# Kernel optimization log

Hardware: AMD Instinct MI355X
Metric: run time of the kernel (lower is better)

The kernel has to match this reference:

```python
import jax, jax.numpy as jnp
import numpy as np

# static config (mirrors init_kwargs)
F_T, S = 8, 24            # video_shape = (F_T, S, S)
K, DIL = 3, 1             # kernel_size, dilation (same for all 3 axes)
HEADS, DHEAD, DIM = 8, 64, 512
INNER = HEADS * DHEAD
PAD = DIL * (K - 1)       # causal: pad 2 at the FRONT of each spatial axis
KJ = K ** 3               # 27 neighbors per query
N_VID = F_T * S * S       # 4608 video tokens


def causal_pad(t):
    # t: [B, D, F, S, S] -> pad front of f/h/w axes (torch F.pad (PAD*?,0) causal layout)
    return jnp.pad(t, ((0, 0), (0, 0), (PAD, 0), (PAD, 0), (PAD, 0)))


def unfold3d(t):
    # torch unfoldNd equivalent. t: [B, D, F+PAD, S+PAD, S+PAD]
    # returns [B, N_VID, KJ, D]; kernel offsets ordered (kf, kh, kw) w fastest,
    # matching torch unfold's channel-major / kernel-minor layout after the
    # rearrange 'b (d j) i -> b i j d'.
    sl = []
    for i in range(K):
        for j in range(K):
            for kk in range(K):
                sl.append(t[:, :, i * DIL:i * DIL + F_T,
                                  j * DIL:j * DIL + S,
                                  kk * DIL:kk * DIL + S])
    u = jnp.stack(sl, axis=2)                      # [B, D, KJ, F, S, S]
    B, D = t.shape[0], t.shape[1]
    u = u.reshape(B, D, KJ, N_VID)
    return jnp.transpose(u, (0, 3, 2, 1))          # [B, N_VID, KJ, D]


def make_mask():
    # True where the neighbor falls into zero padding (out-of-range / future under causal pad)
    ones = jnp.ones((1, 1, F_T, S, S), jnp.float32)
    u = unfold3d(causal_pad(ones))[0, :, :, 0]     # [N_VID, KJ]
    m = u == 0.0
    return jnp.pad(m, ((0, 0), (1, 0)), constant_values=False)  # bos col never masked


def stable_softmax(t, alpha=32.0 ** 2):
    t = t / alpha
    t = t - jax.lax.stop_gradient(jnp.max(t, axis=-1, keepdims=True))
    return jax.nn.softmax(t * alpha, axis=-1)


def setup_inputs() -> dict:
    key = jax.random.key(0)
    ks = jax.random.split(key, 9)
    return {
        "x": jax.random.normal(ks[0], (1, N_VID + 1, DIM), jnp.float32),
        "Wq": jax.random.normal(ks[1], (DIM, INNER), jnp.float32) * 0.02,
        "Wkv": jax.random.normal(ks[2], (DIM, 2 * INNER), jnp.float32) * 0.02,
        "W_th": jax.random.normal(ks[3], (HEADS, HEADS), jnp.float32) * 0.2,
        "Wout": jax.random.normal(ks[4], (INNER, DIM), jnp.float32) * 0.02,
        "bout": jax.random.normal(ks[5], (DIM,), jnp.float32) * 0.02,
        "ax1": jax.random.normal(ks[6], (K, HEADS), jnp.float32),
        "ax2": jax.random.normal(ks[7], (K, HEADS), jnp.float32),
        "ax3": jax.random.normal(ks[8], (K, HEADS), jnp.float32),
    }


def reference(x, Wq, Wkv, W_th, Wout, bout, ax1, ax2, ax3):
    b, n, _ = x.shape                       # b=1, n = 1 + N_VID (no extra padding)
    h, d = HEADS, DHEAD
    scale = d ** -0.5

    q = x @ Wq
    k, v = jnp.split(x @ Wkv, 2, axis=-1)

    def to_heads(t):  # 'b n (h d) -> (b h) n d'
        return t.reshape(b, n, h, d).transpose(0, 2, 1, 3).reshape(b * h, n, d)

    q, k, v = map(to_heads, (q, k, v))
    q = q[:, 1:] * scale                    # drop bos query
    k_bos, v_bos = k[:, :1], v[:, :1]       # [bh, 1, d]
    k, v = k[:, 1:], v[:, 1:]

    def to_vid(t):  # 'b (f h w) d -> b d f h w'
        return t.reshape(b * h, F_T, S, S, d).transpose(0, 4, 1, 2, 3)

    ku = unfold3d(causal_pad(to_vid(k)))    # [bh, N, KJ, d]
    vu = unfold3d(causal_pad(to_vid(v)))
    N = ku.shape[1]

    kb = jnp.broadcast_to(k_bos[:, :, None, :], (b * h, N, 1, d))
    vb = jnp.broadcast_to(v_bos[:, :, None, :], (b * h, N, 1, d))
    ku = jnp.concatenate([kb, ku], axis=2)  # [bh, N, KJ+1, d]
    vu = jnp.concatenate([vb, vu], axis=2)

    sim = jnp.einsum('bid,bijd->bij', q, ku)                 # [bh, N, KJ+1]

    # axial relative position bias over the 3x3x3 kernel, pad 0 for bos column
    rel = (ax1[:, None, None, :] + ax2[None, :, None, :] + ax3[None, None, :, :])
    rel = rel.reshape(KJ, h)                                 # [27, h]
    bias = jnp.pad(rel.T[:, None, :], ((0, 0), (0, 0), (1, 0)))  # [h, 1, KJ+1]

    sim = sim.reshape(b, h, N, KJ + 1) + bias[None]
    mask = make_mask()                                       # [N, KJ+1]
    sim = jnp.where(mask[None, None], -jnp.finfo(sim.dtype).max, sim)

    attn = stable_softmax(sim)                               # [b, h, N, KJ+1]
    attn = jnp.einsum('hg,bgij->bhij', W_th, attn)           # talking heads 1x1 conv

    out = jnp.einsum('bhij,bhijd->bhid', attn, vu.reshape(b, h, N, KJ + 1, d))
    out = jnp.concatenate([v_bos.reshape(b, h, 1, d), out], axis=2)  # re-attach bos value
    out = out.transpose(0, 2, 1, 3).reshape(b, n, h * d)     # '(b h) n d -> b n (h d)'
    return out @ Wout + bout
```

## Files before the change

### kernel.cpp

```cpp
#include <hip/hip_runtime.h>
#include <hip/hip_bf16.h>


constexpr int TFR   = 8;
constexpr int SDIM  = 24;
constexpr int NVID  = TFR * SDIM * SDIM;
constexpr int NTOK  = NVID + 1;
constexpr int NH    = 8;
constexpr int DM    = 512;
constexpr int NJ    = 28;

typedef __attribute__((ext_vector_type(8))) short bf16x8;
typedef __attribute__((ext_vector_type(8))) unsigned short ushort8;
typedef __attribute__((ext_vector_type(4))) float f32x4;

typedef const __attribute__((address_space(1))) unsigned int* gas_ptr;
typedef __attribute__((address_space(3))) unsigned int* las_ptr;

__device__ __forceinline__ float bf2f(unsigned short u) {
    return __uint_as_float((unsigned)u << 16);
}
__device__ __forceinline__ unsigned short f2bf(float f) {
    __hip_bfloat16 h = __float2bfloat16(f);
    return reinterpret_cast<unsigned short&>(h);
}

__global__ __launch_bounds__(256)
void prep_w(const float* __restrict__ Wq, const float* __restrict__ Wkv,
            const float* __restrict__ Wout,
            __hip_bfloat16* __restrict__ Wqkvt, __hip_bfloat16* __restrict__ Woutt)
{
    __shared__ float t[32][33];
    const int tid = threadIdx.x;
    int tb = blockIdx.x;
    const float* W; __hip_bfloat16* Wt; int Nd, tX, rowOff;
    if (tb < 256)      { W = Wq;   Wt = Wqkvt; Nd = 512;  tX = 16; rowOff = 0;   }
    else if (tb < 768) { tb -= 256; W = Wkv;  Wt = Wqkvt; Nd = 1024; tX = 32; rowOff = 512; }
    else               { tb -= 768; W = Wout; Wt = Woutt; Nd = 512;  tX = 16; rowOff = 0;   }
    const int n0 = (tb % tX) * 32, k0 = (tb / tX) * 32;
    const int r  = tid >> 3;
    const int c4 = (tid & 7) * 4;
    const float4 v = *(const float4*)(W + (size_t)(k0 + r) * Nd + n0 + c4);
    t[r][c4 + 0] = v.x; t[r][c4 + 1] = v.y; t[r][c4 + 2] = v.z; t[r][c4 + 3] = v.w;
    __syncthreads();
    #pragma unroll
    for (int j = 0; j < 4; ++j)
        Wt[(size_t)(rowOff + n0 + r) * 512 + k0 + c4 + j] = __float2bfloat16(t[c4 + j][r]);
}

__global__ __launch_bounds__(256)
void gemm_qkv(const float* __restrict__ A, const __hip_bfloat16* __restrict__ Bt,
              float* __restrict__ Cq, __hip_bfloat16* __restrict__ Ckv, int M)
{
    constexpr int BM = 128, BN = 128, BK = 64, PITCH = 72, K = 512;
    __shared__ short As[BM * PITCH];
    __shared__ __align__(16) short Bs[BN * BK];

    const int tid  = threadIdx.x;
    const int m0   = blockIdx.x * BM;
    const int n0   = blockIdx.y * BN;
    const int lane = tid & 63;
    const int wave = tid >> 6;
    const int wm   = (wave >> 1) * 64;
    const int wn   = (wave & 1) * 64;
    const int col  = lane & 15;
    const int quad = lane >> 4;

    f32x4 acc[4][4] = {};

    for (int k0 = 0; k0 < K; k0 += BK) {
        #pragma unroll
        for (int it = 0; it < 4; ++it) {
            const int idx = it * 256 + tid;
            const int r   = idx >> 3;
            const int u   = (idx & 7) ^ (r & 7);
            const __hip_bfloat16* gp = Bt + (size_t)(n0 + r) * K + k0 + u * 8;
            __builtin_amdgcn_global_load_lds(
                (gas_ptr)gp, (las_ptr)&Bs[(it * 256 + wave * 64) * 8], 16, 0, 0);
        }
        #pragma unroll
        for (int r = 0; r < 4; ++r) {
            const int m  = (tid >> 3) + r * 32;
            const int k8 = (tid & 7) * 8;
            const int gm = (m0 + m < M) ? (m0 + m) : (M - 1);
            const float4 f0 = *(const float4*)(A + (size_t)gm * K + k0 + k8);
            const float4 f1 = *(const float4*)(A + (size_t)gm * K + k0 + k8 + 4);
            unsigned short v[8] = { f2bf(f0.x), f2bf(f0.y), f2bf(f0.z), f2bf(f0.w),
                                    f2bf(f1.x), f2bf(f1.y), f2bf(f1.z), f2bf(f1.w) };
            *(ushort8*)(&As[m * PITCH + k8]) = *(const ushort8*)v;
        }
        __syncthreads();

        #pragma unroll
        for (int ks = 0; ks < 2; ++ks) {
            bf16x8 af[4], bfr[4];
            #pragma unroll
            for (int mt = 0; mt < 4; ++mt)
                af[mt] = *(const bf16x8*)(&As[(wm + mt * 16 + col) * PITCH + ks * 32 + quad * 8]);
            #pragma unroll
            for (int nt = 0; nt < 4; ++nt) {
                const int r = wn + nt * 16 + col;
                const int u = (ks * 4 + quad) ^ (r & 7);
                bfr[nt] = *(const bf16x8*)(&Bs[r * BK + u * 8]);
            }
            #pragma unroll
            for (int mt = 0; mt < 4; ++mt)
                #pragma unroll
                for (int nt = 0; nt < 4; ++nt)
                    acc[mt][nt] = __builtin_amdgcn_mfma_f32_16x16x32_bf16(
                        af[mt], bfr[nt], acc[mt][nt], 0, 0, 0);
        }
        __syncthreads();
    }

    const bool isQ = (n0 < 512);
    #pragma unroll
    for (int mt = 0; mt < 4; ++mt) {
        #pragma unroll
        for (int r = 0; r < 4; ++r) {
            const int row = m0 + wm + mt * 16 + quad * 4 + r;
            if (row >= M) continue;
            #pragma unroll
            for (int nt = 0; nt < 4; ++nt) {
                const int cg = n0 + wn + nt * 16 + col;
                const float v = acc[mt][nt][r];
                if (isQ) Cq[(size_t)row * 512 + cg] = v * 0.125f;
                else     Ckv[(size_t)row * 1024 + (cg - 512)] = __float2bfloat16(v);
            }
        }
    }
}

__global__ __launch_bounds__(256)
void gemm_out(const __hip_bfloat16* __restrict__ A, const __hip_bfloat16* __restrict__ Bt,
              float* __restrict__ C, int M, const float* __restrict__ bias)
{
    constexpr int BM = 64, BN = 64, BK = 64, K = 512;
    __shared__ __align__(16) short As[BM * BK];
    __shared__ __align__(16) short Bs[BN * BK];

    const int tid  = threadIdx.x;
    const int m0   = blockIdx.x * BM;
    const int n0   = blockIdx.y * BN;
    const int lane = tid & 63;
    const int wave = tid >> 6;
    const int wm   = (wave >> 1) * 32;
    const int wn   = (wave & 1) * 32;
    const int col  = lane & 15;
    const int quad = lane >> 4;

    f32x4 acc[2][2] = {};

    for (int k0 = 0; k0 < K; k0 += BK) {
        #pragma unroll
        for (int it = 0; it < 2; ++it) {
            const int idx = it * 256 + tid;
            const int r   = idx >> 3;
            const int u   = (idx & 7) ^ (r & 7);
            const __hip_bfloat16* gp = A + (size_t)(m0 + r) * K + k0 + u * 8;
            __builtin_amdgcn_global_load_lds(
                (gas_ptr)gp, (las_ptr)&As[(it * 256 + wave * 64) * 8], 16, 0, 0);
        }
        #pragma unroll
        for (int it = 0; it < 2; ++it) {
            const int idx = it * 256 + tid;
            const int r   = idx >> 3;
            const int u   = (idx & 7) ^ (r & 7);
            const __hip_bfloat16* gp = Bt + (size_t)(n0 + r) * K + k0 + u * 8;
            __builtin_amdgcn_global_load_lds(
                (gas_ptr)gp, (las_ptr)&Bs[(it * 256 + wave * 64) * 8], 16, 0, 0);
        }
        __syncthreads();

        #pragma unroll
        for (int ks = 0; ks < 2; ++ks) {
            bf16x8 af[2], bfr[2];
            #pragma unroll
            for (int mt = 0; mt < 2; ++mt) {
                const int r = wm + mt * 16 + col;
                const int u = (ks * 4 + quad) ^ (r & 7);
                af[mt] = *(const bf16x8*)(&As[r * BK + u * 8]);
            }
            #pragma unroll
            for (int nt = 0; nt < 2; ++nt) {
                const int r = wn + nt * 16 + col;
                const int u = (ks * 4 + quad) ^ (r & 7);
                bfr[nt] = *(const bf16x8*)(&Bs[r * BK + u * 8]);
            }
            #pragma unroll
            for (int mt = 0; mt < 2; ++mt)
                #pragma unroll
                for (int nt = 0; nt < 2; ++nt)
                    acc[mt][nt] = __builtin_amdgcn_mfma_f32_16x16x32_bf16(
                        af[mt], bfr[nt], acc[mt][nt], 0, 0, 0);
        }
        __syncthreads();
    }

    #pragma unroll
    for (int mt = 0; mt < 2; ++mt) {
        #pragma unroll
        for (int r = 0; r < 4; ++r) {
            const int row = m0 + wm + mt * 16 + quad * 4 + r;
            if (row >= M) continue;
            #pragma unroll
            for (int nt = 0; nt < 2; ++nt) {
                const int cg = n0 + wn + nt * 16 + col;
                C[(size_t)row * 512 + cg] = acc[mt][nt][r] + bias[cg];
            }
        }
    }
}

__global__ __launch_bounds__(256)
void attn_v2(const float* __restrict__ Q, const __hip_bfloat16* __restrict__ KVb,
             __hip_bfloat16* __restrict__ O,
             const float* __restrict__ W_th,
             const float* __restrict__ ax1, const float* __restrict__ ax2,
             const float* __restrict__ ax3)
{
    __shared__ float attn_s[4][NH * NJ];
    __shared__ float mixed_s[4][NH * NJ];

    const int tid  = threadIdx.x;
    const int wave = tid >> 6;
    const int lane = tid & 63;
    const int g    = lane >> 3;
    const int s    = lane & 7;
    const int i    = __builtin_amdgcn_readfirstlane(blockIdx.x * 4 + (tid >> 6));
    const int qrow = i + 1;

    const int t  = i / (SDIM * SDIM);
    const int rm = i % (SDIM * SDIM);
    const int y  = rm / SDIM;
    const int x  = rm % SDIM;

    float qf[8];
    {
        const float4 q0 = *(const float4*)(Q + (size_t)qrow * DM + lane * 8);
        const float4 q1 = *(const float4*)(Q + (size_t)qrow * DM + lane * 8 + 4);
        qf[0] = q0.x; qf[1] = q0.y; qf[2] = q0.z; qf[3] = q0.w;
        qf[4] = q1.x; qf[5] = q1.y; qf[6] = q1.z; qf[7] = q1.w;
    }
    float a1[3], a2[3], a3[3];
    #pragma unroll
    for (int d = 0; d < 3; ++d) {
        a1[d] = ax1[d * NH + g];
        a2[d] = ax2[d * NH + g];
        a3[d] = ax3[d * NH + g];
    }

    float sim[NJ];
    #pragma unroll
    for (int j = 0; j < NJ; ++j) {
        int row; bool valid; float bias;
        if (j == 0) { row = 0; valid = true; bias = 0.f; }
        else {
            const int jp = j - 1;
            const int di = jp / 9, dj = (jp / 3) % 3, dk = jp % 3;
            const int tt = t + di - 2, yy = y + dj - 2, xx = x + dk - 2;
            valid = (tt >= 0) && (yy >= 0) && (xx >= 0);
            row = 1 + tt * SDIM * SDIM + yy * SDIM + xx;
            bias = a1[di] + a2[dj] + a3[dk];
        }
        if (valid) {
            const ushort8 kv = *(const ushort8*)(KVb + (size_t)row * 1024 + lane * 8);
            float p = 0.f;
            #pragma unroll
            for (int e = 0; e < 8; ++e) p += bf2f(kv[e]) * qf[e];
            p += __shfl_xor(p, 1);
            p += __shfl_xor(p, 2);
            p += __shfl_xor(p, 4);
            sim[j] = p + bias;
        } else {
            sim[j] = -1e30f;
        }
    }

    float m = -1e30f;
    #pragma unroll
    for (int j = 0; j < NJ; ++j) m = fmaxf(m, sim[j]);
    float ssum = 0.f;
    #pragma unroll
    for (int j = 0; j < NJ; ++j) { sim[j] = __expf(sim[j] - m); ssum += sim[j]; }
    const float inv = 1.f / ssum;
    #pragma unroll
    for (int j = 0; j < NJ; ++j) sim[j] *= inv;

    if (s == 0) {
        #pragma unroll
        for (int u = 0; u < 7; ++u) {
            f32x4 v4 = { sim[4*u], sim[4*u+1], sim[4*u+2], sim[4*u+3] };
            *(f32x4*)(&attn_s[wave][g * NJ + 4 * u]) = v4;
        }
    }
    __syncthreads();

    if (tid < NH * NJ) {
        const int h = tid / NJ, j = tid % NJ;
        #pragma unroll
        for (int q = 0; q < 4; ++q) {
            float acc = 0.f;
            #pragma unroll
            for (int gg = 0; gg < NH; ++gg)
                acc += W_th[h * NH + gg] * attn_s[q][gg * NJ + j];
            mixed_s[q][h * NJ + j] = acc;
        }
    }
    __syncthreads();

    float acc8[8] = {};
    #pragma unroll
    for (int j = 0; j < NJ; ++j) {
        int row; bool valid;
        if (j == 0) { row = 0; valid = true; }
        else {
            const int jp = j - 1;
            const int di = jp / 9, dj = (jp / 3) % 3, dk = jp % 3;
            const int tt = t + di - 2, yy = y + dj - 2, xx = x + dk - 2;
            valid = (tt >= 0) && (yy >= 0) && (xx >= 0);
            row = 1 + tt * SDIM * SDIM + yy * SDIM + xx;
        }
        if (valid) {
            const ushort8 vv = *(const ushort8*)(KVb + (size_t)row * 1024 + 512 + lane * 8);
            const float w = mixed_s[wave][g * NJ + j];
            #pragma unroll
            for (int e = 0; e < 8; ++e) acc8[e] += w * bf2f(vv[e]);
        }
    }

    unsigned short o[8];
    #pragma unroll
    for (int e = 0; e < 8; ++e) o[e] = f2bf(acc8[e]);
    *(ushort8*)(O + (size_t)qrow * DM + lane * 8) = *(const ushort8*)o;

    if (i == 0) {
        const ushort8 vb = *(const ushort8*)(KVb + 512 + lane * 8);
        *(ushort8*)(O + lane * 8) = vb;
    }
}

extern "C" void kernel_launch(void* const* d_in, const int* in_sizes, int n_in,
                              void* d_out, int out_size, void* d_ws, size_t ws_size,
                              hipStream_t stream)
{
    const float* x    = (const float*)d_in[0];
    const float* Wq   = (const float*)d_in[1];
    const float* Wkv  = (const float*)d_in[2];
    const float* W_th = (const float*)d_in[3];
    const float* Wout = (const float*)d_in[4];
    const float* bout = (const float*)d_in[5];
    const float* ax1  = (const float*)d_in[6];
    const float* ax2  = (const float*)d_in[7];
    const float* ax3  = (const float*)d_in[8];
    float* out = (float*)d_out;

    char* p = (char*)d_ws;
    float* Qf = (float*)p;                       p += (size_t)NTOK * DM * 4;
    __hip_bfloat16* KVb   = (__hip_bfloat16*)p;  p += (size_t)NTOK * 2 * DM * 2;
    __hip_bfloat16* Ob    = (__hip_bfloat16*)p;  p += (size_t)NTOK * DM * 2;
    __hip_bfloat16* Wqkvt = (__hip_bfloat16*)p;  p += (size_t)3 * DM * DM * 2;
    __hip_bfloat16* Woutt = (__hip_bfloat16*)p;  p += (size_t)DM * DM * 2;

    const dim3 blk(256);
    const int mtiles128 = (NTOK + 127) / 128;
    const int mtiles64  = (NTOK + 63) / 64;

    prep_w<<<1024, blk, 0, stream>>>(Wq, Wkv, Wout, Wqkvt, Woutt);

    gemm_qkv<<<dim3(mtiles128, 12), blk, 0, stream>>>(x, Wqkvt, Qf, KVb, NTOK);

    attn_v2<<<dim3(NVID / 4), blk, 0, stream>>>(Qf, KVb, Ob, W_th, ax1, ax2, ax3);

    gemm_out<<<dim3(mtiles64, 8), blk, 0, stream>>>(Ob, Woutt, out, NTOK, bout);
}
```

Before: 134.4 us.

## Pre-convert x to bf16 and remap blocks across XCDs for L2 locality

The fp32 input x is now converted to bf16 by extra blocks in the weight-prep kernel, so gemm_qkv can stage A tiles into LDS with direct global-to-LDS loads and the same XOR swizzle used for B, instead of doing per-thread fp32 loads and conversions. All three main kernels switch to a 1D grid whose block IDs are remapped so that consecutive tiles land on the same XCD, aiming for better L2 reuse. gemm_out also gains a row clamp for the partial last tile. The cost is an extra bf16 copy of x written to and read back from global memory, plus hardcoded grid sizes.

```diff
diff --git a/kernel.cpp b/kernel.cpp
--- a/kernel.cpp
+++ b/kernel.cpp
@@ -27,12 +27,26 @@
 
 __global__ __launch_bounds__(256)
 void prep_w(const float* __restrict__ Wq, const float* __restrict__ Wkv,
-            const float* __restrict__ Wout,
-            __hip_bfloat16* __restrict__ Wqkvt, __hip_bfloat16* __restrict__ Woutt)
-{
-    __shared__ float t[32][33];
+            const float* __restrict__ Wout, const float* __restrict__ x,
+            __hip_bfloat16* __restrict__ Wqkvt, __hip_bfloat16* __restrict__ Woutt,
+            __hip_bfloat16* __restrict__ xb)
+{
     const int tid = threadIdx.x;
     int tb = blockIdx.x;
+
+    if (tb >= 1024) {
+        const size_t base = (size_t)(tb - 1024) * 2048 + (size_t)tid * 8;
+        if (base < (size_t)NTOK * DM) {
+            const float4 f0 = *(const float4*)(x + base);
+            const float4 f1 = *(const float4*)(x + base + 4);
+            unsigned short v[8] = { f2bf(f0.x), f2bf(f0.y), f2bf(f0.z), f2bf(f0.w),
+                                    f2bf(f1.x), f2bf(f1.y), f2bf(f1.z), f2bf(f1.w) };
+            *(ushort8*)(xb + base) = *(const ushort8*)v;
+        }
+        return;
+    }
+
+    __shared__ float t[32][33];
     const float* W; __hip_bfloat16* Wt; int Nd, tX, rowOff;
     if (tb < 256)      { W = Wq;   Wt = Wqkvt; Nd = 512;  tX = 16; rowOff = 0;   }
     else if (tb < 768) { tb -= 256; W = Wkv;  Wt = Wqkvt; Nd = 1024; tX = 32; rowOff = 512; }
@@ -49,16 +63,20 @@
 }
 
 __global__ __launch_bounds__(256)
-void gemm_qkv(const float* __restrict__ A, const __hip_bfloat16* __restrict__ Bt,
+void gemm_qkv(const __hip_bfloat16* __restrict__ Ab, const __hip_bfloat16* __restrict__ Bt,
               float* __restrict__ Cq, __hip_bfloat16* __restrict__ Ckv, int M)
 {
-    constexpr int BM = 128, BN = 128, BK = 64, PITCH = 72, K = 512;
-    __shared__ short As[BM * PITCH];
+    constexpr int BM = 128, BN = 128, BK = 64, K = 512;
+    __shared__ __align__(16) short As[BM * BK];
     __shared__ __align__(16) short Bs[BN * BK];
 
     const int tid  = threadIdx.x;
-    const int m0   = blockIdx.x * BM;
-    const int n0   = blockIdx.y * BN;
+    const int bid  = blockIdx.x;
+    const int xcd  = bid & 7, pos = bid >> 3;
+    const int L    = (xcd < 4) ? xcd * 56 + pos : 224 + (xcd - 4) * 55 + pos;
+    const int m0   = (L / 12) * BM;
+    const int n0   = (L % 12) * BN;
+
     const int lane = tid & 63;
     const int wave = tid >> 6;
     const int wm   = (wave >> 1) * 64;
@@ -69,6 +87,16 @@
     f32x4 acc[4][4] = {};
 
     for (int k0 = 0; k0 < K; k0 += BK) {
+        #pragma unroll
+        for (int it = 0; it < 4; ++it) {
+            const int idx = it * 256 + tid;
+            const int r   = idx >> 3;
+            const int u   = (idx & 7) ^ (r & 7);
+            const int gm  = (m0 + r < M) ? (m0 + r) : (M - 1);
+            const __hip_bfloat16* gp = Ab + (size_t)gm * K + k0 + u * 8;
+            __builtin_amdgcn_global_load_lds(
+                (gas_ptr)gp, (las_ptr)&As[(it * 256 + wave * 64) * 8], 16, 0, 0);
+        }
         #pragma unroll
         for (int it = 0; it < 4; ++it) {
             const int idx = it * 256 + tid;
@@ -78,25 +106,17 @@
             __builtin_amdgcn_global_load_lds(
                 (gas_ptr)gp, (las_ptr)&Bs[(it * 256 + wave * 64) * 8], 16, 0, 0);
         }
-        #pragma unroll
-        for (int r = 0; r < 4; ++r) {
-            const int m  = (tid >> 3) + r * 32;
-            const int k8 = (tid & 7) * 8;
-            const int gm = (m0 + m < M) ? (m0 + m) : (M - 1);
-            const float4 f0 = *(const float4*)(A + (size_t)gm * K + k0 + k8);
-            const float4 f1 = *(const float4*)(A + (size_t)gm * K + k0 + k8 + 4);
-            unsigned short v[8] = { f2bf(f0.x), f2bf(f0.y), f2bf(f0.z), f2bf(f0.w),
-                                    f2bf(f1.x), f2bf(f1.y), f2bf(f1.z), f2bf(f1.w) };
-            *(ushort8*)(&As[m * PITCH + k8]) = *(const ushort8*)v;
-        }
         __syncthreads();
 
         #pragma unroll
         for (int ks = 0; ks < 2; ++ks) {
             bf16x8 af[4], bfr[4];
             #pragma unroll
-            for (int mt = 0; mt < 4; ++mt)
-                af[mt] = *(const bf16x8*)(&As[(wm + mt * 16 + col) * PITCH + ks * 32 + quad * 8]);
+            for (int mt = 0; mt < 4; ++mt) {
+                const int r = wm + mt * 16 + col;
+                const int u = (ks * 4 + quad) ^ (r & 7);
+                af[mt] = *(const bf16x8*)(&As[r * BK + u * 8]);
+            }
             #pragma unroll
             for (int nt = 0; nt < 4; ++nt) {
                 const int r = wn + nt * 16 + col;
@@ -140,8 +160,10 @@
     __shared__ __align__(16) short Bs[BN * BK];
 
     const int tid  = threadIdx.x;
-    const int m0   = blockIdx.x * BM;
-    const int n0   = blockIdx.y * BN;
+    const int bid  = blockIdx.x;
+    const int L    = (bid & 7) * 73 + (bid >> 3);
+    const int m0   = (L >> 3) * BM;
+    const int n0   = (L & 7) * BN;
     const int lane = tid & 63;
     const int wave = tid >> 6;
     const int wm   = (wave >> 1) * 32;
@@ -157,7 +179,8 @@
             const int idx = it * 256 + tid;
             const int r   = idx >> 3;
             const int u   = (idx & 7) ^ (r & 7);
-            const __hip_bfloat16* gp = A + (size_t)(m0 + r) * K + k0 + u * 8;
+            const int gm  = (m0 + r < M) ? (m0 + r) : (M - 1);
+            const __hip_bfloat16* gp = A + (size_t)gm * K + k0 + u * 8;
             __builtin_amdgcn_global_load_lds(
                 (gas_ptr)gp, (las_ptr)&As[(it * 256 + wave * 64) * 8], 16, 0, 0);
         }
@@ -227,7 +250,8 @@
     const int lane = tid & 63;
     const int g    = lane >> 3;
     const int s    = lane & 7;
-    const int i    = __builtin_amdgcn_readfirstlane(blockIdx.x * 4 + (tid >> 6));
+    const int bsw  = (blockIdx.x & 7) * (NVID / 4 / 8) + (blockIdx.x >> 3);
+    const int i    = __builtin_amdgcn_readfirstlane(bsw * 4 + (tid >> 6));
     const int qrow = i + 1;
 
     const int t  = i / (SDIM * SDIM);
@@ -361,16 +385,15 @@
     __hip_bfloat16* Ob    = (__hip_bfloat16*)p;  p += (size_t)NTOK * DM * 2;
     __hip_bfloat16* Wqkvt = (__hip_bfloat16*)p;  p += (size_t)3 * DM * DM * 2;
     __hip_bfloat16* Woutt = (__hip_bfloat16*)p;  p += (size_t)DM * DM * 2;
+    __hip_bfloat16* xb    = (__hip_bfloat16*)p;  p += (size_t)NTOK * DM * 2;
 
     const dim3 blk(256);
-    const int mtiles128 = (NTOK + 127) / 128;
-    const int mtiles64  = (NTOK + 63) / 64;
-
-    prep_w<<<1024, blk, 0, stream>>>(Wq, Wkv, Wout, Wqkvt, Woutt);
-
-    gemm_qkv<<<dim3(mtiles128, 12), blk, 0, stream>>>(x, Wqkvt, Qf, KVb, NTOK);
+
+    prep_w<<<2177, blk, 0, stream>>>(Wq, Wkv, Wout, x, Wqkvt, Woutt, xb);
+
+    gemm_qkv<<<444, blk, 0, stream>>>(xb, Wqkvt, Qf, KVb, NTOK);
 
     attn_v2<<<dim3(NVID / 4), blk, 0, stream>>>(Qf, KVb, Ob, W_th, ax1, ax2, ax3);
 
-    gemm_out<<<dim3(mtiles64, 8), blk, 0, stream>>>(Ob, Woutt, out, NTOK, bout);
-}
+    gemm_out<<<584, blk, 0, stream>>>(Ob, Woutt, out, NTOK, bout);
+}
```

After: 131.1 us. -2.4%, faster.
